# Performance work log

Measured on AMD Instinct MI355X. Metric: run time of the kernel, lower is better.

The kernel has to match this reference:

```python
import jax, jax.numpy as jnp
import numpy as np

B, N, C = 1, 2048, 1024
H, D = 16, 64          # num_heads, head_dim
S = 8                  # number of frames; tokens per frame = N // S
NEG_INF = jnp.float32(-1e30)  # stand-in for -inf, numerically safe under jit


def setup_inputs() -> dict:
    key = jax.random.key(0)
    ks = jax.random.split(key, 8)
    x = jax.random.normal(ks[0], (B, N, C), dtype=jnp.float32)
    # tokens grouped contiguously by frame (sorted frame ids)
    frame_ids = jnp.repeat(jnp.arange(S, dtype=jnp.int32), N // S)
    is_hub = jax.random.bernoulli(ks[1], 0.05, (N,))
    adj = jax.random.bernoulli(ks[2], 0.25, (S, S))
    adj = adj.at[jnp.arange(S), jnp.arange(S)].set(True)  # frames always see self
    frame_bias = jax.random.normal(ks[3], (S, S), dtype=jnp.float32) * 0.1
    Wqkv = jax.random.normal(ks[4], (C, 3 * C), dtype=jnp.float32) * 0.02
    bqkv = jnp.zeros((3 * C,), dtype=jnp.float32)
    Wproj = jax.random.normal(ks[5], (C, C), dtype=jnp.float32) * 0.02
    bproj = jnp.zeros((C,), dtype=jnp.float32)
    return {"x": x, "frame_ids": frame_ids, "is_hub": is_hub, "adj": adj,
            "frame_bias": frame_bias, "Wqkv": Wqkv, "bqkv": bqkv,
            "Wproj": Wproj, "bproj": bproj}


def reference(x, frame_ids, is_hub, adj, frame_bias, Wqkv, bqkv, Wproj, bproj):
    # qkv projection: (B,N,3C) -> (3,B,H,N,D)
    qkv = (x @ Wqkv + bqkv).reshape(B, N, 3, H, D).transpose(2, 0, 3, 1, 4)
    q, k, v = qkv[0], qkv[1], qkv[2]

    # flex_attention: scores scaled by 1/sqrt(D) BEFORE score_mod
    scores = jnp.einsum("bhnd,bhmd->bhnm", q, k) * (D ** -0.5)

    # score_mod, vectorized over all (qi,kj) pairs:
    fi = frame_ids                                   # (N,)
    allow = adj[fi][:, fi]                           # (N,N) frame adjacency per token pair
    diff_frame = fi[:, None] != fi[None, :]
    hub_block = diff_frame & (is_hub[:, None] | is_hub[None, :])
    allow = allow & ~hub_block                       # mask_hub_tokens=True
    bias = frame_bias[fi][:, fi]                     # soft_mask=True: add frame-level bias

    scores = jnp.where(allow, scores + bias, NEG_INF)  # broadcast over (b,h)
    attn = jax.nn.softmax(scores, axis=-1)
    out = jnp.einsum("bhnm,bhmd->bhnd", attn, v)
    out = out.transpose(0, 2, 1, 3).reshape(B, N, C)
    return out @ Wproj + bproj
```

## Files before the change

### kernel.cpp

```cpp
#include <hip/hip_runtime.h>

#define NTOK 2048
#define CDIM 1024
#define NHEAD 16
#define HDIM 64
#define NFRM 8
#define FTOK 256

typedef unsigned short ushort;
typedef unsigned long long u64;
typedef __attribute__((ext_vector_type(8))) short short8;
typedef __attribute__((ext_vector_type(8))) ushort ushort8;
typedef __attribute__((ext_vector_type(4))) ushort ushort4v;
typedef __attribute__((ext_vector_type(4))) float floatx4;

__device__ __forceinline__ ushort f2bf(float f) {
    unsigned int u = __float_as_uint(f);
    return (ushort)((u + 0x7fffu + ((u >> 16) & 1u)) >> 16);
}

__device__ __forceinline__ void gload_lds16(const void* g, void* l) {
    __builtin_amdgcn_global_load_lds(
        (const __attribute__((address_space(1))) unsigned int*)(uintptr_t)g,
        (__attribute__((address_space(3))) unsigned int*)(unsigned int)(uintptr_t)l,
        16, 0, 0);
}

__global__ __launch_bounds__(256)
void prep_kernel(const float* __restrict__ x, ushort* __restrict__ xb,
                 const float* __restrict__ Wqkv, ushort* __restrict__ wqkvT,
                 const float* __restrict__ Wproj, ushort* __restrict__ wprojT,
                 const int* __restrict__ is_hub, u64* __restrict__ hubmask)
{
    __shared__ ushort LT[64][72];
    const int b = blockIdx.x, t = threadIdx.x;

    if (b < 2048) {
        int i = b * 256 + t;
        float4 f = ((const float4*)x)[i];
        ushort4v o = { f2bf(f.x), f2bf(f.y), f2bf(f.z), f2bf(f.w) };
        ((ushort4v*)xb)[i] = o;
        return;
    }
    if (b >= 3072) {
        if (t < NTOK / 64) {
            u64 m = 0;
            for (int j = 0; j < 64; ++j)
                m |= (u64)(is_hub[t * 64 + j] != 0) << j;
            hubmask[t] = m;
        }
        return;
    }

    const float* W; ushort* WT; int K, N, n0, k0;
    if (b < 2816) { int idx = b - 2048; W = Wqkv;  WT = wqkvT;  K = 1024; N = 3072;
                    n0 = (idx % 48) * 64; k0 = (idx / 48) * 64; }
    else          { int idx = b - 2816; W = Wproj; WT = wprojT; K = 1024; N = 1024;
                    n0 = (idx & 15) * 64; k0 = (idx >> 4) * 64; }

    const int kr = t >> 4, nc = t & 15;
#pragma unroll
    for (int i = 0; i < 4; ++i) {
        int k = kr + i * 16;
        float4 w4 = *(const float4*)(W + (size_t)(k0 + k) * N + n0 + nc * 4);
        LT[nc*4+0][k] = f2bf(w4.x);
        LT[nc*4+1][k] = f2bf(w4.y);
        LT[nc*4+2][k] = f2bf(w4.z);
        LT[nc*4+3][k] = f2bf(w4.w);
    }
    __syncthreads();
    const int n = t >> 2;
#pragma unroll
    for (int half = 0; half < 2; ++half) {
        int kc = (t & 3) + 4 * half;
        ushort8 v = *(const ushort8*)&LT[n][kc * 8];
        *(ushort8*)(WT + (size_t)(n0 + n) * K + k0 + kc * 8) = v;
    }
}

__global__ __launch_bounds__(256)
void gemm_bt_kernel(const ushort* __restrict__ A, const ushort* __restrict__ BT,
                    const float* __restrict__ bias, void* __restrict__ out,
                    ushort* __restrict__ vtb,
                    int M, int N, int K, int mode)
{
    __shared__ ushort As[2][128 * 32];
    __shared__ ushort Bs[2][128 * 32];

    const int t = threadIdx.x;
    const int wave = t >> 6, lane = t & 63;
    const int quad = lane >> 4, l15 = lane & 15;
    const int row0 = blockIdx.y * 128, col0 = blockIdx.x * 128;
    const int wm = (wave >> 1) * 64, wn = (wave & 1) * 64;

    const int sr = lane >> 2;
    const int sc = (lane & 3) * 8;
    const int r0 = wave * 32;

    floatx4 acc[4][4];
#pragma unroll
    for (int i = 0; i < 4; ++i)
#pragma unroll
        for (int j = 0; j < 4; ++j) acc[i][j] = (floatx4){0.f, 0.f, 0.f, 0.f};

    gload_lds16(A  + (size_t)(row0 + r0      + sr) * K + sc, &As[0][ r0       * 32]);
    gload_lds16(A  + (size_t)(row0 + r0 + 16 + sr) * K + sc, &As[0][(r0 + 16) * 32]);
    gload_lds16(BT + (size_t)(col0 + r0      + sr) * K + sc, &Bs[0][ r0       * 32]);
    gload_lds16(BT + (size_t)(col0 + r0 + 16 + sr) * K + sc, &Bs[0][(r0 + 16) * 32]);

    const int nk = K >> 5;
    for (int ki = 0; ki < nk; ++ki) {
        __syncthreads();
        if (ki + 1 < nk) {
            const int kn = (ki + 1) << 5;
            const int b = (ki + 1) & 1;
            gload_lds16(A  + (size_t)(row0 + r0      + sr) * K + kn + sc, &As[b][ r0       * 32]);
            gload_lds16(A  + (size_t)(row0 + r0 + 16 + sr) * K + kn + sc, &As[b][(r0 + 16) * 32]);
            gload_lds16(BT + (size_t)(col0 + r0      + sr) * K + kn + sc, &Bs[b][ r0       * 32]);
            gload_lds16(BT + (size_t)(col0 + r0 + 16 + sr) * K + kn + sc, &Bs[b][(r0 + 16) * 32]);
        }
        const ushort* as = As[ki & 1];
        const ushort* bs = Bs[ki & 1];

        short8 af[4], bfr[4];
#pragma unroll
        for (int i = 0; i < 4; ++i)
            af[i] = *(const short8*)&as[(wm + i * 16 + l15) * 32 + quad * 8];
#pragma unroll
        for (int j = 0; j < 4; ++j)
            bfr[j] = *(const short8*)&bs[(wn + j * 16 + l15) * 32 + quad * 8];
#pragma unroll
        for (int i = 0; i < 4; ++i)
#pragma unroll
            for (int j = 0; j < 4; ++j)
                acc[i][j] = __builtin_amdgcn_mfma_f32_16x16x32_bf16(af[i], bfr[j], acc[i][j], 0, 0, 0);
    }

    if (mode == 0) {
        float* outf = (float*)out;
#pragma unroll
        for (int j = 0; j < 4; ++j) {
            int col = col0 + wn + j * 16 + l15;
            float bb = bias[col];
#pragma unroll
            for (int i = 0; i < 4; ++i) {
                int rowb = row0 + wm + i * 16 + quad * 4;
#pragma unroll
                for (int r = 0; r < 4; ++r)
                    outf[(size_t)(rowb + r) * N + col] = acc[i][j][r] + bb;
            }
        }
    } else {
        ushort* outb = (ushort*)out;
#pragma unroll
        for (int j = 0; j < 4; ++j) {
            int col = col0 + wn + j * 16 + l15;
            float bb = bias[col];
            int part = col >> 10, hh = (col >> 6) & 15, d = col & 63;
            if (part < 2) {
                ushort* dst = outb + ((size_t)(part * NHEAD + hh) * NTOK) * HDIM + d;
#pragma unroll
                for (int i = 0; i < 4; ++i) {
                    int rowb = row0 + wm + i * 16 + quad * 4;
#pragma unroll
                    for (int r = 0; r < 4; ++r)
                        dst[(size_t)(rowb + r) * HDIM] = f2bf(acc[i][j][r] + bb);
                }
            } else {
                ushort* dst = vtb + ((size_t)hh * HDIM + d) * NTOK;
#pragma unroll
                for (int i = 0; i < 4; ++i) {
                    int rowb = row0 + wm + i * 16 + quad * 4;
#pragma unroll
                    for (int r = 0; r < 4; ++r)
                        dst[rowb + r] = f2bf(acc[i][j][r] + bb);
                }
            }
        }
    }
}

__global__ __launch_bounds__(256)
void attn_tile_kernel(const ushort* __restrict__ qkvb,
                      const ushort* __restrict__ vTb,
                      const int* __restrict__ frame_ids,
                      const u64* __restrict__ hubmask,
                      const int* __restrict__ adj,
                      const float* __restrict__ frame_bias,
                      ushort* __restrict__ attnb)
{
    __shared__ ushort Ks [2][64 * 72];
    __shared__ ushort VTs[2][64 * 72];
    __shared__ ushort Ps [4][16 * 72];

    const int t = threadIdx.x;
    const int wave = t >> 6, lane = t & 63;
    const int quad = lane >> 4, l15 = lane & 15;
    const int b = blockIdx.x;
    const int h = b & 15, q0 = (b >> 4) * 64;

    const ushort* Qg = qkvb + ((size_t)h * NTOK) * HDIM;
    const ushort* Kg = qkvb + ((size_t)(NHEAD + h) * NTOK) * HDIM;
    const ushort* Vg = vTb + ((size_t)h * HDIM) * NTOK;

    short8 aq0 = *(const short8*)(Qg + (size_t)(q0 + wave * 16 + l15) * HDIM + quad * 8);
    short8 aq1 = *(const short8*)(Qg + (size_t)(q0 + wave * 16 + l15) * HDIM + 32 + quad * 8);

    const int fq = frame_ids[q0];
    unsigned vpack = 0; int nv = 0;
#pragma unroll
    for (int f = 0; f < NFRM; ++f)
        if (adj[fq * NFRM + f]) { vpack |= (unsigned)f << (3 * nv); ++nv; }
    const int ntot = nv * 4;

    const u64 hmq = hubmask[q0 >> 6];
    int qh[4];
#pragma unroll
    for (int r = 0; r < 4; ++r) qh[r] = (int)((hmq >> (wave * 16 + quad * 4 + r)) & 1);

    float lpart[4] = {0.f, 0.f, 0.f, 0.f};
    floatx4 oacc[4];
#pragma unroll
    for (int dt = 0; dt < 4; ++dt) oacc[dt] = (floatx4){0.f, 0.f, 0.f, 0.f};

    const int sro = wave * 16 + (lane >> 3);
    const int sc  = (lane & 7) * 8;

    auto tile_k0 = [&](int vt) -> int {
        const int fj = (int)((vpack >> (3 * (vt >> 2))) & 7u);
        return fj * FTOK + (vt & 3) * 64;
    };

    auto stage = [&](int vt) {
        const int k0 = tile_k0(vt);
        const int bf = vt & 1;
        ushort8 k8a = *(const ushort8*)(Kg + (size_t)(k0 + sro)     * HDIM + sc);
        ushort8 k8b = *(const ushort8*)(Kg + (size_t)(k0 + sro + 8) * HDIM + sc);
        ushort8 v8a = *(const ushort8*)(Vg + (size_t)(sro)     * NTOK + k0 + sc);
        ushort8 v8b = *(const ushort8*)(Vg + (size_t)(sro + 8) * NTOK + k0 + sc);
        *(ushort8*)&Ks [bf][ sro      * 72 + sc] = k8a;
        *(ushort8*)&Ks [bf][(sro + 8) * 72 + sc] = k8b;
        *(ushort8*)&VTs[bf][ sro      * 72 + sc] = v8a;
        *(ushort8*)&VTs[bf][(sro + 8) * 72 + sc] = v8b;
    };

    stage(0);

    for (int vt = 0; vt < ntot; ++vt) {
        __syncthreads();

        if (vt + 1 < ntot) stage(vt + 1);

        const int fj = (int)((vpack >> (3 * (vt >> 2))) & 7u);
        const int k0 = fj * FTOK + (vt & 3) * 64;
        const float fb = frame_bias[fq * NFRM + fj];
        const bool same = (fj == fq);
        const u64 hmk = hubmask[k0 >> 6];
        const ushort* ks = Ks[vt & 1];
        const ushort* vs = VTs[vt & 1];

        floatx4 s[4];
#pragma unroll
        for (int nt = 0; nt < 4; ++nt) {
            short8 bk0 = *(const short8*)&ks[(nt * 16 + l15) * 72 + quad * 8];
            short8 bk1 = *(const short8*)&ks[(nt * 16 + l15) * 72 + 32 + quad * 8];
            s[nt] = (floatx4){0.f, 0.f, 0.f, 0.f};
            s[nt] = __builtin_amdgcn_mfma_f32_16x16x32_bf16(aq0, bk0, s[nt], 0, 0, 0);
            s[nt] = __builtin_amdgcn_mfma_f32_16x16x32_bf16(aq1, bk1, s[nt], 0, 0, 0);
        }

#pragma unroll
        for (int r = 0; r < 4; ++r) {
            float ps = 0.f;
#pragma unroll
            for (int nt = 0; nt < 4; ++nt) {
                int kh = (int)((hmk >> (nt * 16 + l15)) & 1);
                bool allow = same || ((qh[r] == 0) && (kh == 0));
                float sv = allow ? fmaf(s[nt][r], 0.125f, fb) : -1.0e30f;
                float p = __expf(sv);
                ps += p;
                Ps[wave][(quad * 4 + r) * 72 + nt * 16 + l15] = f2bf(p);
            }
            lpart[r] += ps;
        }

        short8 ap0 = *(const short8*)&Ps[wave][l15 * 72 + quad * 8];
        short8 ap1 = *(const short8*)&Ps[wave][l15 * 72 + 32 + quad * 8];
#pragma unroll
        for (int dt = 0; dt < 4; ++dt) {
            short8 bv0 = *(const short8*)&vs[(dt * 16 + l15) * 72 + quad * 8];
            short8 bv1 = *(const short8*)&vs[(dt * 16 + l15) * 72 + 32 + quad * 8];
            oacc[dt] = __builtin_amdgcn_mfma_f32_16x16x32_bf16(ap0, bv0, oacc[dt], 0, 0, 0);
            oacc[dt] = __builtin_amdgcn_mfma_f32_16x16x32_bf16(ap1, bv1, oacc[dt], 0, 0, 0);
        }
    }

    float linv[4];
#pragma unroll
    for (int r = 0; r < 4; ++r) {
        float ls = lpart[r];
        ls += __shfl_xor(ls, 1);
        ls += __shfl_xor(ls, 2);
        ls += __shfl_xor(ls, 4);
        ls += __shfl_xor(ls, 8);
        linv[r] = 1.0f / ls;
    }

#pragma unroll
    for (int dt = 0; dt < 4; ++dt) {
        int col = h * HDIM + dt * 16 + l15;
#pragma unroll
        for (int r = 0; r < 4; ++r) {
            int row = q0 + wave * 16 + quad * 4 + r;
            attnb[(size_t)row * CDIM + col] = f2bf(oacc[dt][r] * linv[r]);
        }
    }
}

extern "C" void kernel_launch(void* const* d_in, const int* in_sizes, int n_in,
                              void* d_out, int out_size, void* d_ws, size_t ws_size,
                              hipStream_t stream)
{
    const float* x          = (const float*)d_in[0];
    const int*   frame_ids  = (const int*)d_in[1];
    const int*   is_hub     = (const int*)d_in[2];
    const int*   adj        = (const int*)d_in[3];
    const float* frame_bias = (const float*)d_in[4];
    const float* Wqkv       = (const float*)d_in[5];
    const float* bqkv       = (const float*)d_in[6];
    const float* Wproj      = (const float*)d_in[7];
    const float* bproj      = (const float*)d_in[8];
    float* out = (float*)d_out;

    ushort* xb     = (ushort*)d_ws;
    ushort* wqkvT  = xb     + 2097152;
    ushort* wprojT = wqkvT  + 3145728;
    ushort* qkvb   = wprojT + 1048576;
    ushort* vTb    = qkvb   + 6291456;
    ushort* attnb  = vTb    + 2097152;
    u64*    hubmask = (u64*)(attnb + 2097152);

    prep_kernel<<<dim3(3073), dim3(256), 0, stream>>>(
        x, xb, Wqkv, wqkvT, Wproj, wprojT, is_hub, hubmask);

    gemm_bt_kernel<<<dim3(3 * CDIM / 128, NTOK / 128), dim3(256), 0, stream>>>(
        xb, wqkvT, bqkv, qkvb, vTb, NTOK, 3 * CDIM, CDIM, 1);

    attn_tile_kernel<<<dim3(512), dim3(256), 0, stream>>>(
        qkvb, vTb, frame_ids, hubmask, adj, frame_bias, attnb);

    gemm_bt_kernel<<<dim3(CDIM / 128, NTOK / 128), dim3(256), 0, stream>>>(
        attnb, wprojT, bproj, out, nullptr, NTOK, CDIM, CDIM, 0);
}
```

Measured before the change: 154.3 us.

## Fuse prep, QKV GEMM, attention and projection into one cooperative persistent kernel

Replaces the four separate launches with a single cooperative kernel of 512 blocks that runs the prep, QKV GEMM, attention and output projection phases, separated by grid-wide syncs. The QKV GEMM is retiled to 128x96 so its tiles match the 512 resident blocks, and the projection GEMM uses 64x64 tiles. The attention phase reads V directly from global memory into registers instead of staging it in LDS. This aims to remove launch gaps and tail effects, at the cost of grid.sync overhead and possibly less efficient GEMM tiles. The old multi-kernel path is kept as a fallback when cooperative launch is unavailable.

```diff
diff --git a/kernel.cpp b/kernel.cpp
--- a/kernel.cpp
+++ b/kernel.cpp
@@ -1,4 +1,7 @@
 #include <hip/hip_runtime.h>
+#include <hip/hip_cooperative_groups.h>
+
+namespace cg = cooperative_groups;
 
 #define NTOK 2048
 #define CDIM 1024
@@ -25,6 +28,7 @@
         (__attribute__((address_space(3))) unsigned int*)(unsigned int)(uintptr_t)l,
         16, 0, 0);
 }
+
 
 __global__ __launch_bounds__(256)
 void prep_kernel(const float* __restrict__ x, ushort* __restrict__ xb,
@@ -93,8 +97,7 @@
     const int row0 = blockIdx.y * 128, col0 = blockIdx.x * 128;
     const int wm = (wave >> 1) * 64, wn = (wave & 1) * 64;
 
-    const int sr = lane >> 2;
-    const int sc = (lane & 3) * 8;
+    const int sr = lane >> 2, sc = (lane & 3) * 8;
     const int r0 = wave * 32;
 
     floatx4 acc[4][4];
@@ -248,7 +251,6 @@
 
     for (int vt = 0; vt < ntot; ++vt) {
         __syncthreads();
-
         if (vt + 1 < ntot) stage(vt + 1);
 
         const int fj = (int)((vpack >> (3 * (vt >> 2))) & 7u);
@@ -313,6 +315,333 @@
         for (int r = 0; r < 4; ++r) {
             int row = q0 + wave * 16 + quad * 4 + r;
             attnb[(size_t)row * CDIM + col] = f2bf(oacc[dt][r] * linv[r]);
+        }
+    }
+}
+
+
+struct KParams {
+    const float* x; const int* frame_ids; const int* is_hub; const int* adj;
+    const float* frame_bias; const float* Wqkv; const float* bqkv;
+    const float* Wproj; const float* bproj; float* out;
+    ushort* xb; ushort* wqkvT; ushort* wprojT;
+    ushort* qkvb; ushort* vTb; ushort* attnb; u64* hubmask;
+};
+
+__global__ __launch_bounds__(256)
+void fused_kernel(KParams p)
+{
+    __shared__ ushort SH[14336];
+    cg::grid_group grid = cg::this_grid();
+
+    const int t = threadIdx.x;
+    const int wave = t >> 6, lane = t & 63;
+    const int quad = lane >> 4, l15 = lane & 15;
+
+    for (int u = blockIdx.x; u < 3073; u += 512) {
+        if (u < 2048) {
+            int i = u * 256 + t;
+            float4 f = ((const float4*)p.x)[i];
+            ushort4v o = { f2bf(f.x), f2bf(f.y), f2bf(f.z), f2bf(f.w) };
+            ((ushort4v*)p.xb)[i] = o;
+        } else if (u == 3072) {
+            if (t < NTOK / 64) {
+                u64 m = 0;
+                for (int j = 0; j < 64; ++j)
+                    m |= (u64)(p.is_hub[t * 64 + j] != 0) << j;
+                p.hubmask[t] = m;
+            }
+        } else {
+            ushort (*LT)[72] = (ushort(*)[72])SH;
+            const float* W; ushort* WT; int K, N, n0, k0;
+            if (u < 2816) { int idx = u - 2048; W = p.Wqkv;  WT = p.wqkvT;  K = 1024; N = 3072;
+                            n0 = (idx % 48) * 64; k0 = (idx / 48) * 64; }
+            else          { int idx = u - 2816; W = p.Wproj; WT = p.wprojT; K = 1024; N = 1024;
+                            n0 = (idx & 15) * 64; k0 = (idx >> 4) * 64; }
+            __syncthreads();
+            const int kr = t >> 4, nc = t & 15;
+#pragma unroll
+            for (int i2 = 0; i2 < 4; ++i2) {
+                int k = kr + i2 * 16;
+                float4 w4 = *(const float4*)(W + (size_t)(k0 + k) * N + n0 + nc * 4);
+                LT[nc*4+0][k] = f2bf(w4.x);
+                LT[nc*4+1][k] = f2bf(w4.y);
+                LT[nc*4+2][k] = f2bf(w4.z);
+                LT[nc*4+3][k] = f2bf(w4.w);
+            }
+            __syncthreads();
+            const int n = t >> 2;
+#pragma unroll
+            for (int half = 0; half < 2; ++half) {
+                int kc = (t & 3) + 4 * half;
+                ushort8 v = *(const ushort8*)&LT[n][kc * 8];
+                *(ushort8*)(WT + (size_t)(n0 + n) * K + k0 + kc * 8) = v;
+            }
+        }
+    }
+    grid.sync();
+
+    {
+        const int bx = blockIdx.x & 31, by = blockIdx.x >> 5;
+        const int row0 = by * 128, col0 = bx * 96;
+        const ushort* A  = p.xb;
+        const ushort* BT = p.wqkvT;
+        ushort* As = SH;
+        ushort* Bs = SH + 8192;
+        const int K = 1024;
+        const int sr = lane >> 2, sc = (lane & 3) * 8;
+        const int wm = (wave >> 1) * 64, wn = (wave & 1) * 48;
+
+        floatx4 acc[4][3];
+#pragma unroll
+        for (int i = 0; i < 4; ++i)
+#pragma unroll
+            for (int j = 0; j < 3; ++j) acc[i][j] = (floatx4){0.f, 0.f, 0.f, 0.f};
+
+        auto stage = [&](int buf, int kk) {
+            ushort* as = As + buf * 4096;
+            ushort* bs = Bs + buf * 3072;
+            for (int g = wave; g < 8; g += 4)
+                gload_lds16(A  + (size_t)(row0 + g * 16 + sr) * K + kk + sc, &as[(g * 16) * 32]);
+            for (int g = wave; g < 6; g += 4)
+                gload_lds16(BT + (size_t)(col0 + g * 16 + sr) * K + kk + sc, &bs[(g * 16) * 32]);
+        };
+        stage(0, 0);
+
+        for (int ki = 0; ki < 32; ++ki) {
+            __syncthreads();
+            if (ki + 1 < 32) stage((ki + 1) & 1, (ki + 1) << 5);
+            const ushort* as = As + (ki & 1) * 4096;
+            const ushort* bs = Bs + (ki & 1) * 3072;
+
+            short8 af[4], bfr[3];
+#pragma unroll
+            for (int i = 0; i < 4; ++i)
+                af[i] = *(const short8*)&as[(wm + i * 16 + l15) * 32 + quad * 8];
+#pragma unroll
+            for (int j = 0; j < 3; ++j)
+                bfr[j] = *(const short8*)&bs[(wn + j * 16 + l15) * 32 + quad * 8];
+#pragma unroll
+            for (int i = 0; i < 4; ++i)
+#pragma unroll
+                for (int j = 0; j < 3; ++j)
+                    acc[i][j] = __builtin_amdgcn_mfma_f32_16x16x32_bf16(af[i], bfr[j], acc[i][j], 0, 0, 0);
+        }
+
+#pragma unroll
+        for (int j = 0; j < 3; ++j) {
+            const int colb = col0 + wn + j * 16;
+            const float bb = p.bqkv[colb + l15];
+            const int part = colb >> 10, hh = (colb >> 6) & 15, d0 = colb & 63;
+            if (part < 2) {
+                ushort* dst = p.qkvb + ((size_t)(part * NHEAD + hh) * NTOK) * HDIM + d0 + l15;
+#pragma unroll
+                for (int i = 0; i < 4; ++i) {
+                    int rowb = row0 + wm + i * 16 + quad * 4;
+#pragma unroll
+                    for (int r = 0; r < 4; ++r)
+                        dst[(size_t)(rowb + r) * HDIM] = f2bf(acc[i][j][r] + bb);
+                }
+            } else {
+                ushort* dst = p.vTb + ((size_t)hh * HDIM + d0 + l15) * NTOK;
+#pragma unroll
+                for (int i = 0; i < 4; ++i) {
+                    int rowb = row0 + wm + i * 16 + quad * 4;
+#pragma unroll
+                    for (int r = 0; r < 4; ++r)
+                        dst[rowb + r] = f2bf(acc[i][j][r] + bb);
+                }
+            }
+        }
+    }
+    grid.sync();
+
+    {
+        ushort* Ks0 = SH;
+        ushort* Ks1 = SH + 4608;
+        ushort* Ps  = SH + 9216 + wave * 1152;
+
+        const int b = blockIdx.x;
+        const int h = b & 15, q0 = (b >> 4) * 64;
+
+        const ushort* Qg = p.qkvb + ((size_t)h * NTOK) * HDIM;
+        const ushort* Kg = p.qkvb + ((size_t)(NHEAD + h) * NTOK) * HDIM;
+        const ushort* Vg = p.vTb + ((size_t)h * HDIM) * NTOK;
+
+        short8 aq0 = *(const short8*)(Qg + (size_t)(q0 + wave * 16 + l15) * HDIM + quad * 8);
+        short8 aq1 = *(const short8*)(Qg + (size_t)(q0 + wave * 16 + l15) * HDIM + 32 + quad * 8);
+
+        const int fq = p.frame_ids[q0];
+        unsigned vpack = 0; int nv = 0;
+#pragma unroll
+        for (int f = 0; f < NFRM; ++f)
+            if (p.adj[fq * NFRM + f]) { vpack |= (unsigned)f << (3 * nv); ++nv; }
+        const int ntot = nv * 4;
+
+        const u64 hmq = p.hubmask[q0 >> 6];
+        int qh[4];
+#pragma unroll
+        for (int r = 0; r < 4; ++r) qh[r] = (int)((hmq >> (wave * 16 + quad * 4 + r)) & 1);
+
+        float lpart[4] = {0.f, 0.f, 0.f, 0.f};
+        floatx4 oacc[4];
+#pragma unroll
+        for (int dt = 0; dt < 4; ++dt) oacc[dt] = (floatx4){0.f, 0.f, 0.f, 0.f};
+
+        const int sro = wave * 16 + (lane >> 3);
+        const int scA = (lane & 7) * 8;
+
+        auto tile_k0 = [&](int vt) -> int {
+            const int fj = (int)((vpack >> (3 * (vt >> 2))) & 7u);
+            return fj * FTOK + (vt & 3) * 64;
+        };
+        auto stageK = [&](int vt) {
+            const int k0 = tile_k0(vt);
+            ushort* kd = (vt & 1) ? Ks1 : Ks0;
+            ushort8 k8a = *(const ushort8*)(Kg + (size_t)(k0 + sro)     * HDIM + scA);
+            ushort8 k8b = *(const ushort8*)(Kg + (size_t)(k0 + sro + 8) * HDIM + scA);
+            *(ushort8*)&kd[ sro      * 72 + scA] = k8a;
+            *(ushort8*)&kd[(sro + 8) * 72 + scA] = k8b;
+        };
+
+        __syncthreads();
+        stageK(0);
+
+        for (int vt = 0; vt < ntot; ++vt) {
+            __syncthreads();
+
+            const int fj = (int)((vpack >> (3 * (vt >> 2))) & 7u);
+            const int k0 = fj * FTOK + (vt & 3) * 64;
+            const float fb = p.frame_bias[fq * NFRM + fj];
+            const bool same = (fj == fq);
+            const u64 hmk = p.hubmask[k0 >> 6];
+            const ushort* ks = (vt & 1) ? Ks1 : Ks0;
+
+            short8 bv[4][2];
+#pragma unroll
+            for (int dt = 0; dt < 4; ++dt) {
+                const ushort* vp = Vg + (size_t)(dt * 16 + l15) * NTOK + k0;
+                bv[dt][0] = *(const short8*)(vp + quad * 8);
+                bv[dt][1] = *(const short8*)(vp + 32 + quad * 8);
+            }
+
+            if (vt + 1 < ntot) stageK(vt + 1);
+
+            floatx4 s[4];
+#pragma unroll
+            for (int nt = 0; nt < 4; ++nt) {
+                short8 bk0 = *(const short8*)&ks[(nt * 16 + l15) * 72 + quad * 8];
+                short8 bk1 = *(const short8*)&ks[(nt * 16 + l15) * 72 + 32 + quad * 8];
+                s[nt] = (floatx4){0.f, 0.f, 0.f, 0.f};
+                s[nt] = __builtin_amdgcn_mfma_f32_16x16x32_bf16(aq0, bk0, s[nt], 0, 0, 0);
+                s[nt] = __builtin_amdgcn_mfma_f32_16x16x32_bf16(aq1, bk1, s[nt], 0, 0, 0);
+            }
+
+#pragma unroll
+            for (int r = 0; r < 4; ++r) {
+                float ps = 0.f;
+#pragma unroll
+                for (int nt = 0; nt < 4; ++nt) {
+                    int kh = (int)((hmk >> (nt * 16 + l15)) & 1);
+                    bool allow = same || ((qh[r] == 0) && (kh == 0));
+                    float sv = allow ? fmaf(s[nt][r], 0.125f, fb) : -1.0e30f;
+                    float pv = __expf(sv);
+                    ps += pv;
+                    Ps[(quad * 4 + r) * 72 + nt * 16 + l15] = f2bf(pv);
+                }
+                lpart[r] += ps;
+            }
+
+            short8 ap0 = *(const short8*)&Ps[l15 * 72 + quad * 8];
+            short8 ap1 = *(const short8*)&Ps[l15 * 72 + 32 + quad * 8];
+#pragma unroll
+            for (int dt = 0; dt < 4; ++dt) {
+                oacc[dt] = __builtin_amdgcn_mfma_f32_16x16x32_bf16(ap0, bv[dt][0], oacc[dt], 0, 0, 0);
+                oacc[dt] = __builtin_amdgcn_mfma_f32_16x16x32_bf16(ap1, bv[dt][1], oacc[dt], 0, 0, 0);
+            }
+        }
+
+        float linv[4];
+#pragma unroll
+        for (int r = 0; r < 4; ++r) {
+            float ls = lpart[r];
+            ls += __shfl_xor(ls, 1);
+            ls += __shfl_xor(ls, 2);
+            ls += __shfl_xor(ls, 4);
+            ls += __shfl_xor(ls, 8);
+            linv[r] = 1.0f / ls;
+        }
+
+#pragma unroll
+        for (int dt = 0; dt < 4; ++dt) {
+            int col = h * HDIM + dt * 16 + l15;
+#pragma unroll
+            for (int r = 0; r < 4; ++r) {
+                int row = q0 + wave * 16 + quad * 4 + r;
+                p.attnb[(size_t)row * CDIM + col] = f2bf(oacc[dt][r] * linv[r]);
+            }
+        }
+    }
+    grid.sync();
+
+    {
+        const int bx = blockIdx.x & 15, by = blockIdx.x >> 4;
+        const int row0 = by * 64, col0 = bx * 64;
+        const ushort* A  = p.attnb;
+        const ushort* BT = p.wprojT;
+        ushort* As = SH;
+        ushort* Bs = SH + 4096;
+        const int K = 1024;
+        const int sr = lane >> 2, sc = (lane & 3) * 8;
+        const int wm = (wave >> 1) * 32, wn = (wave & 1) * 32;
+
+        floatx4 acc[2][2];
+#pragma unroll
+        for (int i = 0; i < 2; ++i)
+#pragma unroll
+            for (int j = 0; j < 2; ++j) acc[i][j] = (floatx4){0.f, 0.f, 0.f, 0.f};
+
+        auto stage = [&](int buf, int kk) {
+            ushort* as = As + buf * 2048;
+            ushort* bs = Bs + buf * 2048;
+            gload_lds16(A  + (size_t)(row0 + wave * 16 + sr) * K + kk + sc, &as[(wave * 16) * 32]);
+            gload_lds16(BT + (size_t)(col0 + wave * 16 + sr) * K + kk + sc, &bs[(wave * 16) * 32]);
+        };
+
+        __syncthreads();
+        stage(0, 0);
+
+        for (int ki = 0; ki < 32; ++ki) {
+            __syncthreads();
+            if (ki + 1 < 32) stage((ki + 1) & 1, (ki + 1) << 5);
+            const ushort* as = As + (ki & 1) * 2048;
+            const ushort* bs = Bs + (ki & 1) * 2048;
+
+            short8 af[2], bfr[2];
+#pragma unroll
+            for (int i = 0; i < 2; ++i)
+                af[i] = *(const short8*)&as[(wm + i * 16 + l15) * 32 + quad * 8];
+#pragma unroll
+            for (int j = 0; j < 2; ++j)
+                bfr[j] = *(const short8*)&bs[(wn + j * 16 + l15) * 32 + quad * 8];
+#pragma unroll
+            for (int i = 0; i < 2; ++i)
+#pragma unroll
+                for (int j = 0; j < 2; ++j)
+                    acc[i][j] = __builtin_amdgcn_mfma_f32_16x16x32_bf16(af[i], bfr[j], acc[i][j], 0, 0, 0);
+        }
+
+#pragma unroll
+        for (int j = 0; j < 2; ++j) {
+            int col = col0 + wn + j * 16 + l15;
+            float bb = p.bproj[col];
+#pragma unroll
+            for (int i = 0; i < 2; ++i) {
+                int rowb = row0 + wm + i * 16 + quad * 4;
+#pragma unroll
+                for (int r = 0; r < 4; ++r)
+                    p.out[(size_t)(rowb + r) * CDIM + col] = acc[i][j][r] + bb;
+            }
         }
     }
 }
@@ -340,15 +669,38 @@
     ushort* attnb  = vTb    + 2097152;
     u64*    hubmask = (u64*)(attnb + 2097152);
 
-    prep_kernel<<<dim3(3073), dim3(256), 0, stream>>>(
-        x, xb, Wqkv, wqkvT, Wproj, wprojT, is_hub, hubmask);
-
-    gemm_bt_kernel<<<dim3(3 * CDIM / 128, NTOK / 128), dim3(256), 0, stream>>>(
-        xb, wqkvT, bqkv, qkvb, vTb, NTOK, 3 * CDIM, CDIM, 1);
-
-    attn_tile_kernel<<<dim3(512), dim3(256), 0, stream>>>(
-        qkvb, vTb, frame_ids, hubmask, adj, frame_bias, attnb);
-
-    gemm_bt_kernel<<<dim3(CDIM / 128, NTOK / 128), dim3(256), 0, stream>>>(
-        attnb, wprojT, bproj, out, nullptr, NTOK, CDIM, CDIM, 0);
+    KParams p;
+    p.x = x; p.frame_ids = frame_ids; p.is_hub = is_hub; p.adj = adj;
+    p.frame_bias = frame_bias; p.Wqkv = Wqkv; p.bqkv = bqkv;
+    p.Wproj = Wproj; p.bproj = bproj; p.out = out;
+    p.xb = xb; p.wqkvT = wqkvT; p.wprojT = wprojT;
+    p.qkvb = qkvb; p.vTb = vTb; p.attnb = attnb; p.hubmask = hubmask;
+
+    bool launched = false;
+    int dev = 0;
+    (void)hipGetDevice(&dev);
+    int coopAttr = 0;
+    (void)hipDeviceGetAttribute(&coopAttr, hipDeviceAttributeCooperativeLaunch, dev);
+    int maxBlk = 0;
+    hipError_t qe = hipOccupancyMaxActiveBlocksPerMultiprocessor(
+        &maxBlk, (const void*)fused_kernel, 256, 0);
+    if (coopAttr && qe == hipSuccess && maxBlk >= 2) {
+        void* kargs[] = { (void*)&p };
+        hipError_t le = hipLaunchCooperativeKernel((const void*)fused_kernel,
+                                                   dim3(512), dim3(256),
+                                                   kargs, 0, stream);
+        if (le == hipSuccess) launched = true;
+        else (void)hipGetLastError();
+    }
+
+    if (!launched) {
+        prep_kernel<<<dim3(3073), dim3(256), 0, stream>>>(
+            x, xb, Wqkv, wqkvT, Wproj, wprojT, is_hub, hubmask);
+        gemm_bt_kernel<<<dim3(3 * CDIM / 128, NTOK / 128), dim3(256), 0, stream>>>(
+            xb, wqkvT, bqkv, qkvb, vTb, NTOK, 3 * CDIM, CDIM, 1);
+        attn_tile_kernel<<<dim3(512), dim3(256), 0, stream>>>(
+            qkvb, vTb, frame_ids, hubmask, adj, frame_bias, attnb);
+        gemm_bt_kernel<<<dim3(CDIM / 128, NTOK / 128), dim3(256), 0, stream>>>(
+            attnb, wprojT, bproj, out, nullptr, NTOK, CDIM, CDIM, 0);
+    }
 }
```

New measurement: 155.9 us. About the same (+1.1%).
